# Kernel tuning notes

Hardware: AMD Instinct MI355X
Metric: run time of the kernel (lower is better)

The kernel has to match this reference:

```python
import jax, jax.numpy as jnp
import numpy as np

N_NODES = 100000
N_EDGES = 1600000
F_IN = 64
HID = 128
N_CLASSES = 16
N_GRAPHS = 128


def _glorot(key, shape):
    fan_in = shape[1]
    bound = 1.0 / np.sqrt(fan_in)
    return jax.random.uniform(key, shape, jnp.float32, -bound, bound)


def setup_inputs() -> dict:
    key = jax.random.key(0)
    ks = jax.random.split(key, 12)
    x = jax.random.normal(ks[0], (N_NODES, F_IN), jnp.float32)
    edge_index = jax.random.randint(ks[1], (2, N_EDGES), 0, N_NODES, jnp.int64)
    batch = jnp.sort(jax.random.randint(ks[2], (N_NODES,), 0, N_GRAPHS, jnp.int64))
    # GraphConv l: out = lin_rel(sum_j x_j) + lin_root(x); lin_rel has bias, lin_root does not.
    W1_rel = _glorot(ks[3], (HID, F_IN)); b1 = jnp.zeros((HID,), jnp.float32)
    W1_root = _glorot(ks[4], (HID, F_IN))
    W2_rel = _glorot(ks[5], (HID, HID)); b2 = jnp.zeros((HID,), jnp.float32)
    W2_root = _glorot(ks[6], (HID, HID))
    W3_rel = _glorot(ks[7], (HID, HID)); b3 = jnp.zeros((HID,), jnp.float32)
    W3_root = _glorot(ks[8], (HID, HID))
    W_lin = _glorot(ks[9], (N_CLASSES, HID))
    b_lin = jnp.zeros((N_CLASSES,), jnp.float32)
    return {"x": x, "edge_index": edge_index, "batch": batch,
            "W1_rel": W1_rel, "b1": b1, "W1_root": W1_root,
            "W2_rel": W2_rel, "b2": b2, "W2_root": W2_root,
            "W3_rel": W3_rel, "b3": b3, "W3_root": W3_root,
            "W_lin": W_lin, "b_lin": b_lin}


def graph_conv(x, src, dst, W_rel, b_rel, W_root):
    # gather messages from source nodes, scatter-add at targets
    agg = jax.ops.segment_sum(x[src], dst, num_segments=N_NODES)  # [N, in]
    return agg @ W_rel.T + b_rel + x @ W_root.T


def reference(x, edge_index, batch, W1_rel, b1, W1_root, W2_rel, b2, W2_root,
              W3_rel, b3, W3_root, W_lin, b_lin):
    src, dst = edge_index[0], edge_index[1]
    h = jax.nn.relu(graph_conv(x, src, dst, W1_rel, b1, W1_root))
    h = jax.nn.relu(graph_conv(h, src, dst, W2_rel, b2, W2_root))
    h = graph_conv(h, src, dst, W3_rel, b3, W3_root)
    # global_mean_pool over batch ids
    sums = jax.ops.segment_sum(h, batch, num_segments=N_GRAPHS)  # [G, HID]
    counts = jax.ops.segment_sum(jnp.ones((h.shape[0],), h.dtype), batch,
                                 num_segments=N_GRAPHS)
    pooled = sums / jnp.maximum(counts, 1.0)[:, None]
    # dropout is identity in eval mode
    return pooled @ W_lin.T + b_lin
```

## Files before the change

kernel.cpp:

```cpp
#include <hip/hip_runtime.h>

#define N_NODES_C 100000
#define N_GRAPHS_C 128

typedef __attribute__((ext_vector_type(8))) __bf16 bf16x8;
typedef __attribute__((ext_vector_type(4))) float f32x4;

__device__ __forceinline__ f32x4 mfma16(bf16x8 a, bf16x8 b, f32x4 c) {
    return __builtin_amdgcn_mfma_f32_16x16x32_bf16(a, b, c, 0, 0, 0);
}

__global__ void hist_kernel(const int* __restrict__ ei, int E, int* __restrict__ deg) {
    int i = blockIdx.x * blockDim.x + threadIdx.x;
    if (i < E) atomicAdd(&deg[ei[E + i]], 1);
}

__global__ void scan1_kernel(const int* __restrict__ deg, int N,
                             int* __restrict__ tmp, int* __restrict__ bsum) {
    __shared__ int sh[512];
    int t = threadIdx.x;
    int i = blockIdx.x * 512 + t;
    int v = (i < N) ? deg[i] : 0;
    sh[t] = v;
    __syncthreads();
    for (int off = 1; off < 512; off <<= 1) {
        int add = (t >= off) ? sh[t - off] : 0;
        __syncthreads();
        sh[t] += add;
        __syncthreads();
    }
    if (i < N) tmp[i] = sh[t] - v;
    if (t == 511) bsum[blockIdx.x] = sh[511];
}

__global__ void scan2_kernel(int* bsum, int nb) {
    if (threadIdx.x == 0 && blockIdx.x == 0) {
        int run = 0;
        for (int j = 0; j < nb; ++j) { int v = bsum[j]; bsum[j] = run; run += v; }
    }
}

__global__ void scan3_kernel(const int* __restrict__ tmp, const int* __restrict__ bsum,
                             int N, int* __restrict__ rowp) {
    int i = blockIdx.x * 512 + threadIdx.x;
    if (i < N) rowp[i] = tmp[i] + bsum[blockIdx.x];
}

__global__ void fill_kernel(const int* __restrict__ ei, int E, const int* __restrict__ rowp,
                            int* __restrict__ cursor, int* __restrict__ csr) {
    int i = blockIdx.x * blockDim.x + threadIdx.x;
    if (i < E) {
        int d = ei[E + i];
        int pos = rowp[d] + atomicAdd(&cursor[d], 1);
        csr[pos] = ei[i];
    }
}

template <int FIN>
__global__ __launch_bounds__(256) void agg_kernel(const float* __restrict__ xin,
                                                  const int* __restrict__ rowp,
                                                  const int* __restrict__ degv,
                                                  const int* __restrict__ csrc,
                                                  float* __restrict__ aggout, int nNodes) {
    int wave = blockIdx.x * 4 + (threadIdx.x >> 6);
    int lane = threadIdx.x & 63;
    if (wave >= nNodes) return;
    int start = rowp[wave];
    int deg = degv[wave];
    const float2* xin2 = (const float2*)xin;

    if (FIN == 64) {
        float s[8];
#pragma unroll
        for (int q = 0; q < 8; ++q) s[q] = 0.f;
        for (int base = 0; base < deg; base += 64) {
            int cnt = min(64, deg - base);
            int sid = (lane < cnt) ? csrc[start + base + lane] : 0;
            int j = 0;
            for (; j + 8 <= cnt; j += 8) {
                int n[8];
#pragma unroll
                for (int q = 0; q < 8; ++q) n[q] = __shfl(sid, j + q);
#pragma unroll
                for (int q = 0; q < 8; ++q) s[q] += xin[n[q] * 64 + lane];
            }
            for (; j < cnt; ++j) s[0] += xin[__shfl(sid, j) * 64 + lane];
        }
        aggout[wave * 64 + lane] = ((s[0]+s[1])+(s[2]+s[3])) + ((s[4]+s[5])+(s[6]+s[7]));
    } else {
        float2 a[8];
#pragma unroll
        for (int q = 0; q < 8; ++q) { a[q].x = 0.f; a[q].y = 0.f; }
        for (int base = 0; base < deg; base += 64) {
            int cnt = min(64, deg - base);
            int sid = (lane < cnt) ? csrc[start + base + lane] : 0;
            int j = 0;
            for (; j + 8 <= cnt; j += 8) {
                int n[8];
#pragma unroll
                for (int q = 0; q < 8; ++q) n[q] = __shfl(sid, j + q);
#pragma unroll
                for (int q = 0; q < 8; ++q) {
                    float2 v = xin2[n[q] * 64 + lane];
                    a[q].x += v.x; a[q].y += v.y;
                }
            }
            for (; j < cnt; ++j) {
                float2 v = xin2[__shfl(sid, j) * 64 + lane];
                a[0].x += v.x; a[0].y += v.y;
            }
        }
        float2 o;
        o.x = ((a[0].x+a[1].x)+(a[2].x+a[3].x)) + ((a[4].x+a[5].x)+(a[6].x+a[7].x));
        o.y = ((a[0].y+a[1].y)+(a[2].y+a[3].y)) + ((a[4].y+a[5].y)+(a[6].y+a[7].y));
        ((float2*)aggout)[wave * 64 + lane] = o;
    }
}

__global__ void wprep_kernel(const float* __restrict__ Wrel, const float* __restrict__ Wroot,
                             int KH, unsigned* __restrict__ img) {
    int cid = blockIdx.x;
    int col = threadIdx.x;
    int key = (col >> 1) & 3;
    unsigned hiw[16], low[16];
#pragma unroll 4
    for (int p = 0; p < 16; ++p) {
        int k0 = cid * 32 + p * 2;
        float v0 = (k0 < KH) ? Wrel[col * KH + k0] : Wroot[col * KH + k0 - KH];
        float v1 = (k0 + 1 < KH) ? Wrel[col * KH + k0 + 1] : Wroot[col * KH + k0 + 1 - KH];
        unsigned u0 = __float_as_uint(v0), u1 = __float_as_uint(v1);
        unsigned h0 = u0 & 0xFFFF0000u, h1 = u1 & 0xFFFF0000u;
        float l0 = v0 - __uint_as_float(h0), l1 = v1 - __uint_as_float(h1);
        unsigned lb0 = __float_as_uint(l0) & 0xFFFF0000u;
        unsigned lb1 = __float_as_uint(l1) & 0xFFFF0000u;
        hiw[p] = (h0 >> 16) | h1;
        low[p] = (lb0 >> 16) | lb1;
    }
    unsigned* cb = img + (size_t)cid * 4096;
#pragma unroll 4
    for (int p = 0; p < 16; ++p) {
        int s = p >> 2, w = p & 3;
        int sp = s ^ key;
        cb[col * 16 + sp * 4 + w] = hiw[p];
        cb[2048 + col * 16 + sp * 4 + w] = low[p];
    }
}

template <int KTOT, bool RELU>
__global__ __launch_bounds__(256, 2) void xform_kernel(
    const float* __restrict__ agg, const float* __restrict__ xin,
    const unsigned* __restrict__ wimg, const float* __restrict__ bias,
    float* __restrict__ hout, int nNodes)
{
    constexpr int KH = KTOT / 2;
    constexpr int NC = KTOT / 32;
    __shared__ unsigned sA[2][4096];
    __shared__ unsigned sW[2][4096];
    const int t = threadIdx.x;
    const int nb0 = blockIdx.x * 128;

    const int srow = t >> 1;
    const int skh = t & 1;
    const int skey = (srow >> 1) & 3;
    const int gn = nb0 + srow;
    const bool gvalid = gn < nNodes;
    const size_t arow = (size_t)gn * KH;

    float4 va[4]; uint4 vw[4];
    auto loadChunk = [&](int cix) {
        int kc = cix * 32 + skh * 16;
        const float* srcA = (kc < KH) ? agg : xin;
        int kof = (kc < KH) ? kc : kc - KH;
        if (gvalid) {
#pragma unroll
            for (int q = 0; q < 4; ++q)
                va[q] = *(const float4*)&srcA[arow + kof + q * 4];
        } else {
#pragma unroll
            for (int q = 0; q < 4; ++q) va[q] = make_float4(0.f, 0.f, 0.f, 0.f);
        }
        const uint4* wsrc = (const uint4*)(wimg + (size_t)cix * 4096) + t * 4;
#pragma unroll
        for (int q = 0; q < 4; ++q) vw[q] = wsrc[q];
    };
    auto writeChunk = [&](int buf) {
        uint4* wd = (uint4*)&sW[buf][t * 16];
#pragma unroll
        for (int q = 0; q < 4; ++q) wd[q] = vw[q];
        unsigned hiw[8], low[8];
#pragma unroll
        for (int q = 0; q < 4; ++q) {
            float vv[4] = {va[q].x, va[q].y, va[q].z, va[q].w};
#pragma unroll
            for (int h = 0; h < 2; ++h) {
                unsigned u0 = __float_as_uint(vv[h * 2]), u1 = __float_as_uint(vv[h * 2 + 1]);
                unsigned h0 = u0 & 0xFFFF0000u, h1 = u1 & 0xFFFF0000u;
                float l0 = vv[h * 2] - __uint_as_float(h0);
                float l1 = vv[h * 2 + 1] - __uint_as_float(h1);
                unsigned lb0 = __float_as_uint(l0) & 0xFFFF0000u;
                unsigned lb1 = __float_as_uint(l1) & 0xFFFF0000u;
                hiw[q * 2 + h] = (h0 >> 16) | h1;
                low[q * 2 + h] = (lb0 >> 16) | lb1;
            }
        }
        int s0 = (skh * 2) ^ skey, s1 = (skh * 2 + 1) ^ skey;
        unsigned* abH = &sA[buf][srow * 16];
        unsigned* abL = &sA[buf][2048 + srow * 16];
        *(uint4*)&abH[s0 * 4] = make_uint4(hiw[0], hiw[1], hiw[2], hiw[3]);
        *(uint4*)&abH[s1 * 4] = make_uint4(hiw[4], hiw[5], hiw[6], hiw[7]);
        *(uint4*)&abL[s0 * 4] = make_uint4(low[0], low[1], low[2], low[3]);
        *(uint4*)&abL[s1 * 4] = make_uint4(low[4], low[5], low[6], low[7]);
    };

    const int lane = t & 63, wv = t >> 6;
    const int r15 = lane & 15, hi4 = lane >> 4;
    const int ckey = (r15 >> 1) & 3;
    const int cslot = (hi4 ^ ckey) * 4;
    const int arow0 = (wv * 32 + r15) * 16;
    const int arow1 = arow0 + 256;

    f32x4 acc[2][8];
#pragma unroll
    for (int g = 0; g < 2; ++g)
#pragma unroll
        for (int j = 0; j < 8; ++j) acc[g][j] = (f32x4){0.f, 0.f, 0.f, 0.f};

    float bj[8];
#pragma unroll
    for (int j = 0; j < 8; ++j) bj[j] = bias[j * 16 + r15];

    loadChunk(0);
    writeChunk(0);
    if (NC > 1) loadChunk(1);
    __syncthreads();

#pragma unroll 1
    for (int cix = 0; cix < NC; ++cix) {
        const int cur = cix & 1;
        if (cix + 1 < NC) {
            writeChunk(cur ^ 1);
            if (cix + 2 < NC) loadChunk(cix + 2);
        }
        const unsigned* A = sA[cur];
        const unsigned* W = sW[cur];
        bf16x8 ah0 = *(const bf16x8*)&A[arow0 + cslot];
        bf16x8 ah1 = *(const bf16x8*)&A[arow1 + cslot];
        bf16x8 al0 = *(const bf16x8*)&A[2048 + arow0 + cslot];
        bf16x8 al1 = *(const bf16x8*)&A[2048 + arow1 + cslot];
#pragma unroll
        for (int j = 0; j < 8; ++j) {
            int cb = (j * 16 + r15) * 16;
            bf16x8 bh = *(const bf16x8*)&W[cb + cslot];
            bf16x8 bl = *(const bf16x8*)&W[2048 + cb + cslot];
            acc[0][j] = mfma16(ah0, bh, acc[0][j]);
            acc[1][j] = mfma16(ah1, bh, acc[1][j]);
            acc[0][j] = mfma16(ah0, bl, acc[0][j]);
            acc[1][j] = mfma16(ah1, bl, acc[1][j]);
            acc[0][j] = mfma16(al0, bh, acc[0][j]);
            acc[1][j] = mfma16(al1, bh, acc[1][j]);
        }
        __syncthreads();
    }

#pragma unroll
    for (int g2 = 0; g2 < 2; ++g2) {
#pragma unroll
        for (int r = 0; r < 4; ++r) {
            int node = nb0 + wv * 32 + g2 * 16 + hi4 * 4 + r;
            if (node >= nNodes) continue;
            float* orow = &hout[(size_t)node * 128];
#pragma unroll
            for (int j = 0; j < 8; ++j) {
                float v = acc[g2][j][r] + bj[j];
                if (RELU) v = fmaxf(v, 0.f);
                orow[j * 16 + r15] = v;
            }
        }
    }
}

__global__ void bounds_kernel(const int* __restrict__ batch, int N, int* __restrict__ gstart) {
    int g = blockIdx.x * blockDim.x + threadIdx.x;
    if (g > N_GRAPHS_C) return;
    int lo = 0, hi = N;
    while (lo < hi) {
        int mid = (lo + hi) >> 1;
        if (batch[mid] < g) lo = mid + 1; else hi = mid;
    }
    gstart[g] = lo;
}

__global__ __launch_bounds__(256) void pool2_kernel(const float* __restrict__ h,
                                                    const int* __restrict__ gstart,
                                                    float* __restrict__ pooled) {
    int g = blockIdx.x;
    int f = threadIdx.x & 127;
    int sub = threadIdx.x >> 7;
    int s = gstart[g], e = gstart[g + 1];
    float acc = 0.f;
    for (int n = s + sub; n < e; n += 2) acc += h[(size_t)n * 128 + f];
    __shared__ float sh[128];
    if (sub == 1) sh[f] = acc;
    __syncthreads();
    if (sub == 0) {
        float tot = acc + sh[f];
        float inv = 1.0f / fmaxf((float)(e - s), 1.0f);
        pooled[g * 128 + f] = tot * inv;
    }
}

__global__ void final_kernel(const float* __restrict__ pooled,
                             const float* __restrict__ Wlin, const float* __restrict__ blin,
                             float* __restrict__ out) {
    int idx = blockIdx.x * blockDim.x + threadIdx.x;
    int g = idx >> 4, c = idx & 15;
    float s = 0.f;
    for (int k = 0; k < 128; ++k) s += pooled[g * 128 + k] * Wlin[c * 128 + k];
    out[idx] = s + blin[c];
}

extern "C" void kernel_launch(void* const* d_in, const int* in_sizes, int n_in,
                              void* d_out, int out_size, void* d_ws, size_t ws_size,
                              hipStream_t stream) {
    const float* x      = (const float*)d_in[0];
    const int*   ei     = (const int*)d_in[1];
    const int*   batch  = (const int*)d_in[2];
    const float* W1_rel = (const float*)d_in[3];
    const float* b1     = (const float*)d_in[4];
    const float* W1_root= (const float*)d_in[5];
    const float* W2_rel = (const float*)d_in[6];
    const float* b2     = (const float*)d_in[7];
    const float* W2_root= (const float*)d_in[8];
    const float* W3_rel = (const float*)d_in[9];
    const float* b3     = (const float*)d_in[10];
    const float* W3_root= (const float*)d_in[11];
    const float* W_lin  = (const float*)d_in[12];
    const float* b_lin  = (const float*)d_in[13];
    float* out = (float*)d_out;

    const int N = in_sizes[2];
    const int E = in_sizes[1] / 2;
    const int nb = (N + 511) / 512;

    char* base = (char*)d_ws;
    size_t off = 0;
    auto carve = [&](size_t bytes) -> void* {
        void* p = base + off;
        off = (off + bytes + 255) & ~(size_t)255;
        return p;
    };
    int*      deg    = (int*)carve((size_t)N * 4);
    int*      tmp    = (int*)carve((size_t)N * 4);
    int*      bsum   = (int*)carve(1024);
    int*      rowp   = (int*)carve((size_t)(N + 1) * 4);
    int*      cursor = (int*)carve((size_t)N * 4);
    int*      csr    = (int*)carve((size_t)E * 4);
    float*    aggbuf = (float*)carve((size_t)N * 128 * 4);
    float*    hA     = (float*)carve((size_t)N * 128 * 4);
    float*    hB     = (float*)carve((size_t)N * 128 * 4);
    float*    pooled = (float*)carve((size_t)N_GRAPHS_C * 128 * 4);
    int*      gstart = (int*)carve((size_t)(N_GRAPHS_C + 1) * 4);
    unsigned* wimg1  = (unsigned*)carve((size_t)4 * 4096 * 4);
    unsigned* wimg2  = (unsigned*)carve((size_t)8 * 4096 * 4);
    unsigned* wimg3  = (unsigned*)carve((size_t)8 * 4096 * 4);
    (void)ws_size;

    hipMemsetAsync(deg, 0, (size_t)N * 4, stream);
    hipMemsetAsync(cursor, 0, (size_t)N * 4, stream);

    wprep_kernel<<<4, 128, 0, stream>>>(W1_rel, W1_root, 64, wimg1);
    wprep_kernel<<<8, 128, 0, stream>>>(W2_rel, W2_root, 128, wimg2);
    wprep_kernel<<<8, 128, 0, stream>>>(W3_rel, W3_root, 128, wimg3);

    hist_kernel<<<(E + 255) / 256, 256, 0, stream>>>(ei, E, deg);
    scan1_kernel<<<nb, 512, 0, stream>>>(deg, N, tmp, bsum);
    scan2_kernel<<<1, 64, 0, stream>>>(bsum, nb);
    scan3_kernel<<<nb, 512, 0, stream>>>(tmp, bsum, N, rowp);
    fill_kernel<<<(E + 255) / 256, 256, 0, stream>>>(ei, E, rowp, cursor, csr);

    bounds_kernel<<<1, 192, 0, stream>>>(batch, N, gstart);

    const int aggGrid = (N + 3) / 4;
    const int xGrid = (N + 127) / 128;

    agg_kernel<64><<<aggGrid, 256, 0, stream>>>(x, rowp, deg, csr, aggbuf, N);
    xform_kernel<128, true><<<xGrid, 256, 0, stream>>>(aggbuf, x, wimg1, b1, hA, N);

    agg_kernel<128><<<aggGrid, 256, 0, stream>>>(hA, rowp, deg, csr, aggbuf, N);
    xform_kernel<256, true><<<xGrid, 256, 0, stream>>>(aggbuf, hA, wimg2, b2, hB, N);

    agg_kernel<128><<<aggGrid, 256, 0, stream>>>(hB, rowp, deg, csr, aggbuf, N);
    xform_kernel<256, false><<<xGrid, 256, 0, stream>>>(aggbuf, hB, wimg3, b3, hA, N);

    pool2_kernel<<<N_GRAPHS_C, 256, 0, stream>>>(hA, gstart, pooled);
    final_kernel<<<8, 256, 0, stream>>>(pooled, W_lin, b_lin, out);
}
```

Before: 827.3 us.

## Use float4 multi-edge gathers in aggregation, drop cursor memset, widen pooling loads

The aggregation kernel now has each wave process 2 (FIN=128) or 4 (FIN=64) edges at once, with each lane group loading a float4 slice of a neighbor row. Partial sums are combined with cross-lane xor shuffles before a float4 store. This is meant to raise memory-level parallelism and use wider loads in the gather, which dominates runtime. The CSR fill now atomically bumps a copy of the row pointers, which removes the cursor buffer and its memset, and it writes with nontemporal stores. Pooling uses float4 loads across 8 row subgroups. The costs are extra shuffle reductions and more idle lanes in the tail loop.

```diff
diff --git a/kernel.cpp b/kernel.cpp
--- a/kernel.cpp
+++ b/kernel.cpp
@@ -41,18 +41,22 @@
 }
 
 __global__ void scan3_kernel(const int* __restrict__ tmp, const int* __restrict__ bsum,
-                             int N, int* __restrict__ rowp) {
+                             int N, int* __restrict__ rowp, int* __restrict__ rowpm) {
     int i = blockIdx.x * 512 + threadIdx.x;
-    if (i < N) rowp[i] = tmp[i] + bsum[blockIdx.x];
-}
-
-__global__ void fill_kernel(const int* __restrict__ ei, int E, const int* __restrict__ rowp,
-                            int* __restrict__ cursor, int* __restrict__ csr) {
+    if (i < N) {
+        int v = tmp[i] + bsum[blockIdx.x];
+        rowp[i] = v;
+        rowpm[i] = v;
+    }
+}
+
+__global__ void fill_kernel(const int* __restrict__ ei, int E,
+                            int* __restrict__ rowpm, int* __restrict__ csr) {
     int i = blockIdx.x * blockDim.x + threadIdx.x;
     if (i < E) {
         int d = ei[E + i];
-        int pos = rowp[d] + atomicAdd(&cursor[d], 1);
-        csr[pos] = ei[i];
+        int pos = atomicAdd(&rowpm[d], 1);
+        __builtin_nontemporal_store(ei[i], &csr[pos]);
     }
 }
 
@@ -67,54 +71,59 @@
     if (wave >= nNodes) return;
     int start = rowp[wave];
     int deg = degv[wave];
-    const float2* xin2 = (const float2*)xin;
-
+    const float4* x4 = (const float4*)xin;
+    constexpr int EPW = (FIN == 128) ? 2 : 4;
+    constexpr int RS = FIN / 4;
+    const int grp = lane / RS;
+    const int f4 = lane & (RS - 1);
+
+    float4 acc[8];
+#pragma unroll
+    for (int q = 0; q < 8; ++q) acc[q] = make_float4(0.f, 0.f, 0.f, 0.f);
+
+    for (int base = 0; base < deg; base += 64) {
+        int cnt = min(64, deg - base);
+        int sid = (lane < cnt) ? csrc[start + base + lane] : 0;
+        int j = 0;
+        for (; j + 8 * EPW <= cnt; j += 8 * EPW) {
+            int n[8];
+#pragma unroll
+            for (int q = 0; q < 8; ++q) n[q] = __shfl(sid, j + q * EPW + grp);
+            float4 v[8];
+#pragma unroll
+            for (int q = 0; q < 8; ++q) v[q] = x4[(size_t)n[q] * RS + f4];
+#pragma unroll
+            for (int q = 0; q < 8; ++q) {
+                acc[q].x += v[q].x; acc[q].y += v[q].y;
+                acc[q].z += v[q].z; acc[q].w += v[q].w;
+            }
+        }
+        for (; j + EPW <= cnt; j += EPW) {
+            int n0 = __shfl(sid, j + grp);
+            float4 v = x4[(size_t)n0 * RS + f4];
+            acc[0].x += v.x; acc[0].y += v.y; acc[0].z += v.z; acc[0].w += v.w;
+        }
+        for (; j < cnt; ++j) {
+            int n0 = __shfl(sid, j);
+            if (grp == 0) {
+                float4 v = x4[(size_t)n0 * RS + f4];
+                acc[0].x += v.x; acc[0].y += v.y; acc[0].z += v.z; acc[0].w += v.w;
+            }
+        }
+    }
+    float4 tot;
+    tot.x = ((acc[0].x+acc[1].x)+(acc[2].x+acc[3].x)) + ((acc[4].x+acc[5].x)+(acc[6].x+acc[7].x));
+    tot.y = ((acc[0].y+acc[1].y)+(acc[2].y+acc[3].y)) + ((acc[4].y+acc[5].y)+(acc[6].y+acc[7].y));
+    tot.z = ((acc[0].z+acc[1].z)+(acc[2].z+acc[3].z)) + ((acc[4].z+acc[5].z)+(acc[6].z+acc[7].z));
+    tot.w = ((acc[0].w+acc[1].w)+(acc[2].w+acc[3].w)) + ((acc[4].w+acc[5].w)+(acc[6].w+acc[7].w));
     if (FIN == 64) {
-        float s[8];
-#pragma unroll
-        for (int q = 0; q < 8; ++q) s[q] = 0.f;
-        for (int base = 0; base < deg; base += 64) {
-            int cnt = min(64, deg - base);
-            int sid = (lane < cnt) ? csrc[start + base + lane] : 0;
-            int j = 0;
-            for (; j + 8 <= cnt; j += 8) {
-                int n[8];
-#pragma unroll
-                for (int q = 0; q < 8; ++q) n[q] = __shfl(sid, j + q);
-#pragma unroll
-                for (int q = 0; q < 8; ++q) s[q] += xin[n[q] * 64 + lane];
-            }
-            for (; j < cnt; ++j) s[0] += xin[__shfl(sid, j) * 64 + lane];
-        }
-        aggout[wave * 64 + lane] = ((s[0]+s[1])+(s[2]+s[3])) + ((s[4]+s[5])+(s[6]+s[7]));
-    } else {
-        float2 a[8];
-#pragma unroll
-        for (int q = 0; q < 8; ++q) { a[q].x = 0.f; a[q].y = 0.f; }
-        for (int base = 0; base < deg; base += 64) {
-            int cnt = min(64, deg - base);
-            int sid = (lane < cnt) ? csrc[start + base + lane] : 0;
-            int j = 0;
-            for (; j + 8 <= cnt; j += 8) {
-                int n[8];
-#pragma unroll
-                for (int q = 0; q < 8; ++q) n[q] = __shfl(sid, j + q);
-#pragma unroll
-                for (int q = 0; q < 8; ++q) {
-                    float2 v = xin2[n[q] * 64 + lane];
-                    a[q].x += v.x; a[q].y += v.y;
-                }
-            }
-            for (; j < cnt; ++j) {
-                float2 v = xin2[__shfl(sid, j) * 64 + lane];
-                a[0].x += v.x; a[0].y += v.y;
-            }
-        }
-        float2 o;
-        o.x = ((a[0].x+a[1].x)+(a[2].x+a[3].x)) + ((a[4].x+a[5].x)+(a[6].x+a[7].x));
-        o.y = ((a[0].y+a[1].y)+(a[2].y+a[3].y)) + ((a[4].y+a[5].y)+(a[6].y+a[7].y));
-        ((float2*)aggout)[wave * 64 + lane] = o;
-    }
+        tot.x += __shfl_xor(tot.x, 16); tot.y += __shfl_xor(tot.y, 16);
+        tot.z += __shfl_xor(tot.z, 16); tot.w += __shfl_xor(tot.w, 16);
+    }
+    tot.x += __shfl_xor(tot.x, 32); tot.y += __shfl_xor(tot.y, 32);
+    tot.z += __shfl_xor(tot.z, 32); tot.w += __shfl_xor(tot.w, 32);
+    if (lane < RS)
+        ((float4*)aggout)[(size_t)wave * RS + lane] = tot;
 }
 
 __global__ void wprep_kernel(const float* __restrict__ Wrel, const float* __restrict__ Wroot,
@@ -294,18 +303,28 @@
                                                     const int* __restrict__ gstart,
                                                     float* __restrict__ pooled) {
     int g = blockIdx.x;
-    int f = threadIdx.x & 127;
-    int sub = threadIdx.x >> 7;
+    int f4 = threadIdx.x & 31;
+    int sub = threadIdx.x >> 5;
     int s = gstart[g], e = gstart[g + 1];
-    float acc = 0.f;
-    for (int n = s + sub; n < e; n += 2) acc += h[(size_t)n * 128 + f];
-    __shared__ float sh[128];
-    if (sub == 1) sh[f] = acc;
+    const float4* h4 = (const float4*)h;
+    float4 acc = make_float4(0.f, 0.f, 0.f, 0.f);
+    for (int n = s + sub; n < e; n += 8) {
+        float4 v = h4[(size_t)n * 32 + f4];
+        acc.x += v.x; acc.y += v.y; acc.z += v.z; acc.w += v.w;
+    }
+    __shared__ float4 sh[8][33];
+    sh[sub][f4] = acc;
     __syncthreads();
     if (sub == 0) {
-        float tot = acc + sh[f];
+        float4 tot = acc;
+#pragma unroll
+        for (int q = 1; q < 8; ++q) {
+            float4 v = sh[q][f4];
+            tot.x += v.x; tot.y += v.y; tot.z += v.z; tot.w += v.w;
+        }
         float inv = 1.0f / fmaxf((float)(e - s), 1.0f);
-        pooled[g * 128 + f] = tot * inv;
+        tot.x *= inv; tot.y *= inv; tot.z *= inv; tot.w *= inv;
+        ((float4*)pooled)[g * 32 + f4] = tot;
     }
 }
 
@@ -353,7 +372,7 @@
     int*      tmp    = (int*)carve((size_t)N * 4);
     int*      bsum   = (int*)carve(1024);
     int*      rowp   = (int*)carve((size_t)(N + 1) * 4);
-    int*      cursor = (int*)carve((size_t)N * 4);
+    int*      rowpm  = (int*)carve((size_t)N * 4);
     int*      csr    = (int*)carve((size_t)E * 4);
     float*    aggbuf = (float*)carve((size_t)N * 128 * 4);
     float*    hA     = (float*)carve((size_t)N * 128 * 4);
@@ -366,7 +385,6 @@
     (void)ws_size;
 
     hipMemsetAsync(deg, 0, (size_t)N * 4, stream);
-    hipMemsetAsync(cursor, 0, (size_t)N * 4, stream);
 
     wprep_kernel<<<4, 128, 0, stream>>>(W1_rel, W1_root, 64, wimg1);
     wprep_kernel<<<8, 128, 0, stream>>>(W2_rel, W2_root, 128, wimg2);
@@ -375,8 +393,8 @@
     hist_kernel<<<(E + 255) / 256, 256, 0, stream>>>(ei, E, deg);
     scan1_kernel<<<nb, 512, 0, stream>>>(deg, N, tmp, bsum);
     scan2_kernel<<<1, 64, 0, stream>>>(bsum, nb);
-    scan3_kernel<<<nb, 512, 0, stream>>>(tmp, bsum, N, rowp);
-    fill_kernel<<<(E + 255) / 256, 256, 0, stream>>>(ei, E, rowp, cursor, csr);
+    scan3_kernel<<<nb, 512, 0, stream>>>(tmp, bsum, N, rowp, rowpm);
+    fill_kernel<<<(E + 255) / 256, 256, 0, stream>>>(ei, E, rowpm, csr);
 
     bounds_kernel<<<1, 192, 0, stream>>>(batch, N, gstart);
 
```

Result: slower. 845.1 us (+2.2%).
